# Kernel optimization log

Measured on AMD Instinct MI355X. Metric: run time of the kernel, lower is better.

The kernel has to match this reference:

```python
import jax, jax.numpy as jnp
import numpy as np

N_NODES = 4096
D_FEAT = 256


def _interp_linear_2x(x):
    # Matches F.interpolate(mode='linear', scale_factor=2, align_corners=False)
    # applied along the node axis. x: [N, D] -> [2N, D]
    n = x.shape[0]
    out_i = jnp.arange(2 * n, dtype=jnp.float32)
    src = jnp.clip((out_i + 0.5) * 0.5 - 0.5, 0.0, float(n - 1))
    i0 = jnp.floor(src).astype(jnp.int32)
    i1 = jnp.minimum(i0 + 1, n - 1)
    w = (src - i0.astype(jnp.float32))[:, None]
    return x[i0] * (1.0 - w) + x[i1] * w


def _nearest_neighbor_idx(x):
    # argmin over pairwise Euclidean distances with diagonal excluded.
    # Squared distances give the same argmin as torch.cdist.
    sq = jnp.sum(x * x, axis=1)
    d2 = sq[:, None] + sq[None, :] - 2.0 * (x @ x.T)  # [2N, 2N]
    m = x.shape[0]
    d2 = jnp.where(jnp.eye(m, dtype=bool), jnp.inf, d2)
    return jnp.argmin(d2, axis=1)


def setup_inputs() -> dict:
    key = jax.random.key(0)
    k1, k2, k3, k4 = jax.random.split(key, 4)
    x = jax.random.normal(k1, (N_NODES, D_FEAT), dtype=jnp.float32)
    adj = jax.random.uniform(k2, (N_NODES, N_NODES), dtype=jnp.float32)
    # Xavier-uniform-ish init for the two GCN weights
    lim = float(np.sqrt(6.0 / (D_FEAT + D_FEAT)))
    W1 = jax.random.uniform(k3, (D_FEAT, D_FEAT), jnp.float32, -lim, lim)
    W2 = jax.random.uniform(k4, (D_FEAT, D_FEAT), jnp.float32, -lim, lim)
    return {"x": x, "adj": adj, "W1": W1, "W2": W2}


def reference(x, adj, W1, W2):
    # conv1: adj @ (x @ W1)
    h = adj @ (x @ W1)                      # [N, D]
    x2 = _interp_linear_2x(h)               # [2N, D]
    # nearest-neighbor one-hot adjacency, then conv2.
    # one_hot(nn_idx) @ support == support[nn_idx] (exact same math)
    nn_idx = _nearest_neighbor_idx(x2)      # [2N]
    support = x2 @ W2                       # [2N, D]
    return support[nn_idx]                  # [2N, D]
```

## Files before the change

kernel.cpp:

```cpp
#include <hip/hip_runtime.h>
#include <hip/hip_bf16.h>
#include <cstdint>

typedef __attribute__((ext_vector_type(8))) __bf16 bf16x8;
typedef __attribute__((ext_vector_type(4))) float f32x4;

static __device__ __forceinline__ unsigned short f2bf(float f) {
  return __builtin_bit_cast(unsigned short, (__bf16)f);
}
static __device__ __forceinline__ unsigned pack2(float a, float b) {
  return (unsigned)f2bf(a) | ((unsigned)f2bf(b) << 16);
}
#define GLDS(src, dst) __builtin_amdgcn_global_load_lds( \
    (const __attribute__((address_space(1))) void*)(src), \
    (__attribute__((address_space(3))) void*)(dst), 16, 0, 0)


__global__ void transpose_w_kernel(const float* __restrict__ W1, const float* __restrict__ W2,
                                   unsigned short* __restrict__ W1t, unsigned short* __restrict__ W2t) {
  int i = blockIdx.x * 256 + threadIdx.x;
  int k = i >> 8, n = i & 255;
  W1t[n * 256 + k] = f2bf(W1[k * 256 + n]);
  W2t[n * 256 + k] = f2bf(W2[k * 256 + n]);
}

__global__ void upsample_kernel(const unsigned short* __restrict__ hs,
                                unsigned short* __restrict__ x2b, float* __restrict__ sq) {
  int row = blockIdx.x * 4 + (threadIdx.x >> 6);
  int c = (threadIdx.x & 63) * 4;
  float s = (row + 0.5f) * 0.5f - 0.5f;
  s = fminf(fmaxf(s, 0.0f), 4095.0f);
  float fl = floorf(s);
  int i0 = (int)fl;
  int i1 = min((int)fl + 1, 4095);
  float w = s - fl;
  float v0[4] = {0.f, 0.f, 0.f, 0.f}, v1[4] = {0.f, 0.f, 0.f, 0.f};
  #pragma unroll
  for (int k = 0; k < 8; ++k) {
    ushort4 u0 = *(const ushort4*)&hs[(size_t)k * 4096 * 256 + i0 * 256 + c];
    ushort4 u1 = *(const ushort4*)&hs[(size_t)k * 4096 * 256 + i1 * 256 + c];
    v0[0] += __builtin_bit_cast(float, (unsigned)u0.x << 16);
    v0[1] += __builtin_bit_cast(float, (unsigned)u0.y << 16);
    v0[2] += __builtin_bit_cast(float, (unsigned)u0.z << 16);
    v0[3] += __builtin_bit_cast(float, (unsigned)u0.w << 16);
    v1[0] += __builtin_bit_cast(float, (unsigned)u1.x << 16);
    v1[1] += __builtin_bit_cast(float, (unsigned)u1.y << 16);
    v1[2] += __builtin_bit_cast(float, (unsigned)u1.z << 16);
    v1[3] += __builtin_bit_cast(float, (unsigned)u1.w << 16);
  }
  float p = 0.f;
  ushort4 st;
  unsigned short* sp = (unsigned short*)&st;
  #pragma unroll
  for (int e = 0; e < 4; ++e) {
    float v = v0[e] * (1.0f - w) + v1[e] * w;
    sp[e] = f2bf(v);
    p += v * v;
  }
  *(ushort4*)&x2b[(size_t)row * 256 + c] = st;
  #pragma unroll
  for (int m = 32; m > 0; m >>= 1) p += __shfl_down(p, m, 64);
  if ((threadIdx.x & 63) == 0) sq[row] = p;
}

__launch_bounds__(256, 3)
__global__ void gram_kernel(const unsigned short* __restrict__ X,
                            const float* __restrict__ sq,
                            unsigned* __restrict__ pv) {
  __shared__ alignas(16) unsigned short As[128 * 64];
  __shared__ alignas(16) unsigned short Bs[128 * 64];
  __shared__ unsigned mrgr[2][128];
  __shared__ unsigned mrgc[2][128];

  const int tid = threadIdx.x;
  const int wid = tid >> 6;
  const int lane = tid & 63;
  const int g = lane >> 4, lr = lane & 15;
  const int wr = wid >> 1, wc = wid & 1;

  int t = blockIdx.x;
  int bi = (int)((sqrtf(8.0f * (float)t + 1.0f) - 1.0f) * 0.5f);
  while ((bi + 1) * (bi + 2) / 2 <= t) ++bi;
  while (bi * (bi + 1) / 2 > t) --bi;
  const int bx = bi;
  const int by = t - bi * (bi + 1) / 2;
  const int m0 = bx * 128;
  const int n0 = by * 128;
  const bool diag = (bx == by);

  const int srow = tid >> 3;
  const int ssc = (tid & 7) ^ (srow & 7);
  const unsigned short* aBase = X + (size_t)(m0 + srow) * 256 + ssc * 8;
  const unsigned short* bBase = X + (size_t)(n0 + srow) * 256 + ssc * 8;
  unsigned short* const aDst = As + (size_t)(tid >> 6) * 512;
  unsigned short* const bDst = Bs + (size_t)(tid >> 6) * 512;
  const unsigned short* const Bsrc = diag ? As : Bs;

  f32x4 acc[4][4];
  const f32x4 fzero = {0.f, 0.f, 0.f, 0.f};
  #pragma unroll
  for (int i = 0; i < 4; ++i)
    #pragma unroll
    for (int j = 0; j < 4; ++j) acc[i][j] = fzero;

  #pragma unroll
  for (int ks = 0; ks < 4; ++ks) {
    #pragma unroll
    for (int it = 0; it < 4; ++it)
      GLDS(aBase + it * 8192 + ks * 64, aDst + it * 2048);
    if (!diag) {
      #pragma unroll
      for (int it = 0; it < 4; ++it)
        GLDS(bBase + it * 8192 + ks * 64, bDst + it * 2048);
    }
    __syncthreads();
    #pragma unroll
    for (int kk = 0; kk < 2; ++kk) {
      const int ch = (kk * 4 + g) ^ (lr & 7);
      bf16x8 b[4];
      #pragma unroll
      for (int j = 0; j < 4; ++j)
        b[j] = *(const bf16x8*)&Bsrc[(wc * 64 + j * 16 + lr) * 64 + ch * 8];
      #pragma unroll
      for (int i = 0; i < 4; ++i) {
        bf16x8 a = *(const bf16x8*)&As[(wr * 64 + i * 16 + lr) * 64 + ch * 8];
        #pragma unroll
        for (int j = 0; j < 4; ++j)
          acc[i][j] = __builtin_amdgcn_mfma_f32_16x16x32_bf16(a, b[j], acc[i][j], 0, 0, 0);
      }
    }
    __syncthreads();
  }

  int jcol[4];
  float sqj[4];
  unsigned ckey[4];
  #pragma unroll
  for (int j = 0; j < 4; ++j) {
    jcol[j] = n0 + wc * 64 + j * 16 + lr;
    sqj[j] = sq[jcol[j]];
    ckey[j] = 0xFFFFFFFFu;
  }
  #pragma unroll
  for (int i = 0; i < 4; ++i) {
    #pragma unroll
    for (int r = 0; r < 4; ++r) {
      const int lrow = wr * 64 + i * 16 + g * 4 + r;
      const int irow = m0 + lrow;
      const float sqi = sq[irow];
      unsigned rk = 0xFFFFFFFFu;
      #pragma unroll
      for (int j = 0; j < 4; ++j) {
        float v = fmaf(-2.0f, acc[i][j][r], sqi + sqj[j]);
        unsigned bits = __float_as_uint(v) & 0xFFFFE000u;
        unsigned krow = bits | (unsigned)jcol[j];
        if (diag && jcol[j] == irow) krow = 0xFFFFFFFFu;
        rk = min(rk, krow);
        if (!diag) ckey[j] = min(ckey[j], bits | (unsigned)irow);
      }
      #pragma unroll
      for (int m = 1; m < 16; m <<= 1)
        rk = min(rk, (unsigned)__shfl_xor((int)rk, m, 64));
      if (lr == 0) mrgr[wc][lrow] = rk;
    }
  }
  if (!diag) {
    #pragma unroll
    for (int j = 0; j < 4; ++j) {
      ckey[j] = min(ckey[j], (unsigned)__shfl_xor((int)ckey[j], 16, 64));
      ckey[j] = min(ckey[j], (unsigned)__shfl_xor((int)ckey[j], 32, 64));
      if (g == 0) mrgc[wr][wc * 64 + j * 16 + lr] = ckey[j];
    }
  }
  __syncthreads();
  if (tid < 128) {
    pv[(size_t)by * 8192 + m0 + tid] = min(mrgr[0][tid], mrgr[1][tid]);
  } else if (!diag) {
    int c = tid - 128;
    pv[(size_t)(64 + bx) * 8192 + n0 + c] = min(mrgc[0][c], mrgc[1][c]);
  }
}

template <int BM, int BN, int WAVES_M, int KT, int EPI, bool AF32, bool GATHER>
__launch_bounds__(256)
__global__ void gemm_nt_kernel(const void* __restrict__ Ap, int lda,
                               const unsigned short* __restrict__ Bp, int ldb,
                               int M, int N,
                               float* __restrict__ Cf,
                               unsigned short* __restrict__ Cb,
                               const unsigned* __restrict__ pv) {
  constexpr int BK = 64;
  constexpr int NT = KT / BK;
  constexpr int WAVES_N = 4 / WAVES_M;
  constexpr int WM = BM / WAVES_M;
  constexpr int WN = BN / WAVES_N;
  constexpr int FM = WM / 16;
  constexpr int FN = WN / 16;
  constexpr int ASLOT = BM * 8;
  constexpr int AITER = (ASLOT + 255) / 256;
  constexpr int BITER = (BN * 8) / 256;

  __shared__ alignas(16) unsigned short As[BM * BK];
  __shared__ alignas(16) unsigned short Bs[BN * BK];
  __shared__ unsigned redp[GATHER ? 4 * 64 : 1];
  __shared__ unsigned pckl[GATHER ? 64 : 1];

  const int tid = threadIdx.x;
  const int wid = tid >> 6;
  const int lane = tid & 63;
  const int g = lane >> 4;
  const int lr = lane & 15;
  const int wr = wid / WAVES_N;
  const int wc = wid % WAVES_N;
  const int m0 = blockIdx.x * BM;
  const int n0 = blockIdx.y * BN;
  const int kbase = (EPI == 3) ? blockIdx.z * KT : 0;
  if constexpr (EPI == 3) Cb += (size_t)blockIdx.z * (size_t)M * (size_t)N;

  if constexpr (GATHER) {
    static_assert(!GATHER || BM == 64, "inline reduce assumes BM==64");
    const int row = tid & 63;
    const int part = tid >> 6;
    const int cr = m0 >> 7;
    unsigned best = 0xFFFFFFFFu;
    #pragma unroll
    for (int s8 = 0; s8 < 16; ++s8) {
      int s = part * 16 + s8;
      int slot = s + (s > cr ? 64 : 0);
      best = min(best, pv[(size_t)slot * 8192 + m0 + row]);
    }
    redp[part * 64 + row] = best;
    __syncthreads();
    if (tid < 64)
      pckl[tid] = min(min(redp[tid], redp[64 + tid]),
                      min(redp[128 + tid], redp[192 + tid])) & 0x1FFFu;
    __syncthreads();
  }

  const int srow = tid >> 3;
  const int ssc = (tid & 7) ^ (srow & 7);
  const float* aBF[AITER];
  const unsigned short* aBH[AITER];
  #pragma unroll
  for (int it = 0; it < AITER; ++it) {
    int r = m0 + srow + it * 32;
    if constexpr (AF32) {
      aBF[it] = (const float*)Ap + (size_t)r * (size_t)lda + kbase + ssc * 8;
    } else {
      int sr = GATHER ? (int)pckl[srow + it * 32] : r;
      aBH[it] = (const unsigned short*)Ap + (size_t)sr * (size_t)lda + kbase + ssc * 8;
    }
  }
  const unsigned short* bBase = Bp + (size_t)(n0 + srow) * (size_t)ldb + kbase + ssc * 8;
  unsigned short* const sDst = As + (size_t)wid * 512;
  unsigned short* const bDst = Bs + (size_t)wid * 512;

  f32x4 acc[FM][FN];
  const f32x4 fzero = {0.f, 0.f, 0.f, 0.f};
  #pragma unroll
  for (int i = 0; i < FM; ++i)
    #pragma unroll
    for (int j = 0; j < FN; ++j) acc[i][j] = fzero;

  #pragma unroll
  for (int t = 0; t < NT; ++t) {
    #pragma unroll
    for (int it = 0; it < BITER; ++it)
      GLDS(bBase + (size_t)it * 32 * ldb + t * 64, bDst + it * 2048);
    if constexpr (AF32) {
      #pragma unroll
      for (int it = 0; it < AITER; ++it) {
        if (ASLOT % 256 == 0 || it * 256 + tid < ASLOT) {
          const float* src = aBF[it] + t * 64;
          float4 f0 = *(const float4*)src;
          float4 f1 = *(const float4*)(src + 4);
          uint4 pk = { pack2(f0.x, f0.y), pack2(f0.z, f0.w),
                       pack2(f1.x, f1.y), pack2(f1.z, f1.w) };
          *(uint4*)&As[(it * 32 + srow) * BK + (tid & 7) * 8] = pk;
        }
      }
    } else {
      #pragma unroll
      for (int it = 0; it < AITER; ++it)
        GLDS(aBH[it] + t * 64, sDst + it * 2048);
    }
    __syncthreads();
    #pragma unroll
    for (int kk = 0; kk < 2; ++kk) {
      const int ch = (kk * 4 + g) ^ (lr & 7);
      bf16x8 a[FM], b[FN];
      #pragma unroll
      for (int i = 0; i < FM; ++i)
        a[i] = *(const bf16x8*)&As[(wr * WM + i * 16 + lr) * BK + ch * 8];
      #pragma unroll
      for (int j = 0; j < FN; ++j)
        b[j] = *(const bf16x8*)&Bs[(wc * WN + j * 16 + lr) * BK + ch * 8];
      #pragma unroll
      for (int i = 0; i < FM; ++i)
        #pragma unroll
        for (int j = 0; j < FN; ++j)
          acc[i][j] = __builtin_amdgcn_mfma_f32_16x16x32_bf16(a[i], b[j], acc[i][j], 0, 0, 0);
    }
    __syncthreads();
  }

  const int rowb = wr * WM;
  const int colb = wc * WN;
  if constexpr (EPI == 0) {
    #pragma unroll
    for (int i = 0; i < FM; ++i) {
      int mrow = m0 + rowb + i * 16 + g * 4;
      #pragma unroll
      for (int j = 0; j < FN; ++j) {
        int col = n0 + colb + j * 16 + lr;
        #pragma unroll
        for (int r = 0; r < 4; ++r)
          Cf[(size_t)(mrow + r) * N + col] = acc[i][j][r];
      }
    }
  } else if constexpr (EPI == 1) {
    #pragma unroll
    for (int i = 0; i < FM; ++i) {
      int mrow = m0 + rowb + i * 16 + g * 4;
      #pragma unroll
      for (int j = 0; j < FN; ++j) {
        int col = n0 + colb + j * 16 + lr;
        ushort4 st;
        st.x = f2bf(acc[i][j][0]);
        st.y = f2bf(acc[i][j][1]);
        st.z = f2bf(acc[i][j][2]);
        st.w = f2bf(acc[i][j][3]);
        *(ushort4*)&Cb[(size_t)col * M + mrow] = st;
      }
    }
  } else {
    #pragma unroll
    for (int i = 0; i < FM; ++i) {
      int mrow = m0 + rowb + i * 16 + g * 4;
      #pragma unroll
      for (int j = 0; j < FN; ++j) {
        int col = n0 + colb + j * 16 + lr;
        #pragma unroll
        for (int r = 0; r < 4; ++r)
          Cb[(size_t)(mrow + r) * N + col] = f2bf(acc[i][j][r]);
      }
    }
  }
}


extern "C" void kernel_launch(void* const* d_in, const int* in_sizes, int n_in,
                              void* d_out, int out_size, void* d_ws, size_t ws_size,
                              hipStream_t stream) {
  (void)in_sizes; (void)n_in; (void)out_size; (void)ws_size;
  const float* x   = (const float*)d_in[0];
  const float* adj = (const float*)d_in[1];
  const float* W1  = (const float*)d_in[2];
  const float* W2  = (const float*)d_in[3];
  float* out = (float*)d_out;

  char* p = (char*)d_ws;
  unsigned short* Tt  = (unsigned short*)p;  p += 4096 * 256 * 2;
  char* R             = p;                   p += 16 * 1024 * 1024;
  unsigned short* x2b = (unsigned short*)p;  p += 8192 * 256 * 2;
  float* sqv          = (float*)p;           p += 8192 * 4;
  unsigned short* W1t = (unsigned short*)p;  p += 256 * 256 * 2;
  unsigned short* W2t = (unsigned short*)p;  p += 256 * 256 * 2;

  unsigned short* hs = (unsigned short*)R;
  unsigned* pv       = (unsigned*)R;

  transpose_w_kernel<<<256, 256, 0, stream>>>(W1, W2, W1t, W2t);

  gemm_nt_kernel<64, 64, 4, 256, 1, true, false><<<dim3(64, 4), 256, 0, stream>>>(
      x, 256, W1t, 256, 4096, 256, nullptr, Tt, nullptr);

  gemm_nt_kernel<128, 128, 2, 512, 3, true, false><<<dim3(32, 2, 8), 256, 0, stream>>>(
      adj, 4096, Tt, 4096, 4096, 256, nullptr, hs, nullptr);

  upsample_kernel<<<2048, 256, 0, stream>>>(hs, x2b, sqv);

  gram_kernel<<<2080, 256, 0, stream>>>(x2b, sqv, pv);

  gemm_nt_kernel<64, 64, 4, 256, 0, false, true><<<dim3(128, 4), 256, 0, stream>>>(
      x2b, 256, W2t, 256, 8192, 256, out, nullptr, pv);
}
```

Measured before the change: 89.65 us.

## Add dedicated 256x256 split-K adj GEMM kernel and swizzle gram tile order

Replaces the generic split-K gemm for adj@T with a dedicated 512-thread kernel that computes a 256-row by full 256-column tile per block. Each adj row is loaded and converted to bf16 once rather than twice across the two N-tiles, which cuts global traffic on the large fp32 adj matrix. The gram kernel's triangular tile index is also remapped so consecutive blocks are spread across the triangle, which may help cache locality and load balance. The trade-off is a grid of only 128 blocks, each with many accumulators, so occupancy and latency hiding may suffer.

Measured after the change: 98.81 us. 10.2% more time.

```diff
diff --git a/kernel.cpp b/kernel.cpp
--- a/kernel.cpp
+++ b/kernel.cpp
@@ -63,6 +63,88 @@
   if ((threadIdx.x & 63) == 0) sq[row] = p;
 }
 
+__launch_bounds__(512)
+__global__ void adj_gemm_kernel(const float* __restrict__ adjp,
+                                const unsigned short* __restrict__ Ttp,
+                                unsigned short* __restrict__ hs) {
+  constexpr int NT = 8;
+  __shared__ alignas(16) unsigned short As[256 * 64];
+  __shared__ alignas(16) unsigned short Bs[256 * 64];
+
+  const int tid = threadIdx.x;
+  const int wid = tid >> 6;
+  const int lane = tid & 63;
+  const int g = lane >> 4, lr = lane & 15;
+  const int wr = wid >> 2;
+  const int wc = wid & 3;
+  const int m0 = blockIdx.x * 256;
+  const int kbase = blockIdx.y * 512;
+  unsigned short* outp = hs + (size_t)blockIdx.y * 4096 * 256;
+
+  const int srow = tid >> 3;
+  const int scp = tid & 7;
+  const int ssc = scp ^ (srow & 7);
+  const float* aB[4];
+  const unsigned short* bB[4];
+  #pragma unroll
+  for (int it = 0; it < 4; ++it) {
+    aB[it] = adjp + (size_t)(m0 + it * 64 + srow) * 4096 + kbase + ssc * 8;
+    bB[it] = Ttp + (size_t)(it * 64 + srow) * 4096 + kbase + ssc * 8;
+  }
+
+  f32x4 acc[8][4];
+  const f32x4 fzero = {0.f, 0.f, 0.f, 0.f};
+  #pragma unroll
+  for (int i = 0; i < 8; ++i)
+    #pragma unroll
+    for (int j = 0; j < 4; ++j) acc[i][j] = fzero;
+
+  #pragma unroll
+  for (int t = 0; t < NT; ++t) {
+    #pragma unroll
+    for (int it = 0; it < 4; ++it)
+      GLDS(bB[it] + t * 64, Bs + (size_t)(it * 512 + wid * 64) * 8);
+    #pragma unroll
+    for (int it = 0; it < 4; ++it) {
+      const float* src = aB[it] + t * 64;
+      float4 f0 = *(const float4*)src;
+      float4 f1 = *(const float4*)(src + 4);
+      uint4 pk = { pack2(f0.x, f0.y), pack2(f0.z, f0.w),
+                   pack2(f1.x, f1.y), pack2(f1.z, f1.w) };
+      *(uint4*)&As[(it * 64 + srow) * 64 + scp * 8] = pk;
+    }
+    __syncthreads();
+    #pragma unroll
+    for (int kk = 0; kk < 2; ++kk) {
+      const int ch = (kk * 4 + g) ^ (lr & 7);
+      bf16x8 b[4];
+      #pragma unroll
+      for (int j = 0; j < 4; ++j)
+        b[j] = *(const bf16x8*)&Bs[(wc * 64 + j * 16 + lr) * 64 + ch * 8];
+      #pragma unroll
+      for (int i = 0; i < 8; ++i) {
+        bf16x8 a = *(const bf16x8*)&As[(wr * 128 + i * 16 + lr) * 64 + ch * 8];
+        #pragma unroll
+        for (int j = 0; j < 4; ++j)
+          acc[i][j] = __builtin_amdgcn_mfma_f32_16x16x32_bf16(a, b[j], acc[i][j], 0, 0, 0);
+      }
+    }
+    __syncthreads();
+  }
+
+  #pragma unroll
+  for (int i = 0; i < 8; ++i) {
+    int mrow = m0 + wr * 128 + i * 16 + g * 4;
+    #pragma unroll
+    for (int j = 0; j < 4; ++j) {
+      int col = wc * 64 + j * 16 + lr;
+      #pragma unroll
+      for (int r = 0; r < 4; ++r)
+        outp[(size_t)(mrow + r) * 256 + col] = f2bf(acc[i][j][r]);
+    }
+  }
+}
+
 __launch_bounds__(256, 3)
 __global__ void gram_kernel(const unsigned short* __restrict__ X,
                             const float* __restrict__ sq,
@@ -78,7 +160,8 @@
   const int g = lane >> 4, lr = lane & 15;
   const int wr = wid >> 1, wc = wid & 1;
 
-  int t = blockIdx.x;
+  int t0 = blockIdx.x;
+  int t = (t0 & 7) * 260 + (t0 >> 3);
   int bi = (int)((sqrtf(8.0f * (float)t + 1.0f) - 1.0f) * 0.5f);
   while ((bi + 1) * (bi + 2) / 2 <= t) ++bi;
   while (bi * (bi + 1) / 2 > t) --bi;
@@ -214,8 +297,6 @@
   const int wc = wid % WAVES_N;
   const int m0 = blockIdx.x * BM;
   const int n0 = blockIdx.y * BN;
-  const int kbase = (EPI == 3) ? blockIdx.z * KT : 0;
-  if constexpr (EPI == 3) Cb += (size_t)blockIdx.z * (size_t)M * (size_t)N;
 
   if constexpr (GATHER) {
     static_assert(!GATHER || BM == 64, "inline reduce assumes BM==64");
@@ -245,13 +326,13 @@
   for (int it = 0; it < AITER; ++it) {
     int r = m0 + srow + it * 32;
     if constexpr (AF32) {
-      aBF[it] = (const float*)Ap + (size_t)r * (size_t)lda + kbase + ssc * 8;
+      aBF[it] = (const float*)Ap + (size_t)r * (size_t)lda + ssc * 8;
     } else {
       int sr = GATHER ? (int)pckl[srow + it * 32] : r;
-      aBH[it] = (const unsigned short*)Ap + (size_t)sr * (size_t)lda + kbase + ssc * 8;
-    }
-  }
-  const unsigned short* bBase = Bp + (size_t)(n0 + srow) * (size_t)ldb + kbase + ssc * 8;
+      aBH[it] = (const unsigned short*)Ap + (size_t)sr * (size_t)lda + ssc * 8;
+    }
+  }
+  const unsigned short* bBase = Bp + (size_t)(n0 + srow) * (size_t)ldb + ssc * 8;
   unsigned short* const sDst = As + (size_t)wid * 512;
   unsigned short* const bDst = Bs + (size_t)wid * 512;
 
@@ -318,7 +399,7 @@
           Cf[(size_t)(mrow + r) * N + col] = acc[i][j][r];
       }
     }
-  } else if constexpr (EPI == 1) {
+  } else {
     #pragma unroll
     for (int i = 0; i < FM; ++i) {
       int mrow = m0 + rowb + i * 16 + g * 4;
@@ -331,18 +412,6 @@
         st.z = f2bf(acc[i][j][2]);
         st.w = f2bf(acc[i][j][3]);
         *(ushort4*)&Cb[(size_t)col * M + mrow] = st;
-      }
-    }
-  } else {
-    #pragma unroll
-    for (int i = 0; i < FM; ++i) {
-      int mrow = m0 + rowb + i * 16 + g * 4;
-      #pragma unroll
-      for (int j = 0; j < FN; ++j) {
-        int col = n0 + colb + j * 16 + lr;
-        #pragma unroll
-        for (int r = 0; r < 4; ++r)
-          Cb[(size_t)(mrow + r) * N + col] = f2bf(acc[i][j][r]);
       }
     }
   }
@@ -375,8 +444,7 @@
   gemm_nt_kernel<64, 64, 4, 256, 1, true, false><<<dim3(64, 4), 256, 0, stream>>>(
       x, 256, W1t, 256, 4096, 256, nullptr, Tt, nullptr);
 
-  gemm_nt_kernel<128, 128, 2, 512, 3, true, false><<<dim3(32, 2, 8), 256, 0, stream>>>(
-      adj, 4096, Tt, 4096, 4096, 256, nullptr, hs, nullptr);
+  adj_gemm_kernel<<<dim3(16, 8), 512, 0, stream>>>(adj, Tt, hs);
 
   upsample_kernel<<<2048, 256, 0, stream>>>(hs, x2b, sqv);
 
```
